# Performance work log

Measured on AMD Instinct MI355X. Metric: run time of the kernel, lower is better.

The kernel has to match this reference:

```python
import jax, jax.numpy as jnp
import numpy as np
from jax import lax

# ---- static config (matches init_kwargs: input_shape=(1,64,64), num_classes=2) ----
C, H, W = 1, 64, 64
NUM_CLASSES = 2
DIM_CAPS = 8          # primary capsule dim
NUM_PRIM = 32         # primary capsule types
OUT_DIM = 16          # class capsule dim
NUM_ROUTING = 3
HP = (H - 9) // 2 + 1  # 28  (9x9 conv, stride 2, no pad)
WP = (W - 9) // 2 + 1  # 28
IN_CAPS = NUM_PRIM * HP * WP  # 25088
TEMP_CH = 256 // H    # 4  channels after re-viewing temporal output
B = 32


def conv1d(x, w, b, pad):
    y = lax.conv_general_dilated(x, w, (1,), [(pad, pad)],
                                 dimension_numbers=('NCH', 'OIH', 'NCH'))
    return y + b[None, :, None]


def conv2d(x, w, b, stride, pad):
    y = lax.conv_general_dilated(x, w, (stride, stride), [(pad, pad), (pad, pad)],
                                 dimension_numbers=('NCHW', 'OIHW', 'NCHW'))
    return y + b[None, :, None, None]


def squash_vec(u):
    # proper capsule squash over last (dim_caps) axis -- used by PrimaryCapsule
    sn = jnp.sum(u * u, axis=-1, keepdims=True)
    return sn * u / ((1.0 + sn) * jnp.sqrt(sn + 1e-8))


def squash_elem(v):
    # RoutingCapsule squash: torch applies it over a trailing SINGLETON dim,
    # so it is elementwise: v^2 * v / ((1+v^2) * sqrt(v^2 + 1e-8))
    sn = v * v
    return sn * v / ((1.0 + sn) * jnp.sqrt(sn + 1e-8))


def setup_inputs() -> dict:
    key = jax.random.key(0)
    ks = jax.random.split(key, 20)
    s = 0.05
    inp = {
        'x':    jax.random.normal(ks[0], (B, C, H, W), dtype=jnp.float32),
        # temporal Conv1d stack (true in_channels = C*H = 64)
        'w_t1': jax.random.normal(ks[1], (64, C * H, 5), jnp.float32) * s,
        'b_t1': jnp.zeros((64,), jnp.float32),
        'w_t2': jax.random.normal(ks[2], (128, 64, 5), jnp.float32) * s,
        'b_t2': jnp.zeros((128,), jnp.float32),
        'w_t3': jax.random.normal(ks[3], (256, 128, 5), jnp.float32) * s,
        'b_t3': jnp.zeros((256,), jnp.float32),
        # spectral Conv2d stack
        'w_s1': jax.random.normal(ks[4], (64, C, 3, 3), jnp.float32) * s,
        'b_s1': jnp.zeros((64,), jnp.float32),
        'w_s2': jax.random.normal(ks[5], (128, 64, 3, 3), jnp.float32) * s,
        'b_s2': jnp.zeros((128,), jnp.float32),
        'w_s3': jax.random.normal(ks[6], (256, 128, 3, 3), jnp.float32) * s,
        'b_s3': jnp.zeros((256,), jnp.float32),
        # fusion 1x1 conv (in = 256/H + 256 = 260)
        'w_f':  jax.random.normal(ks[7], (256, TEMP_CH + 256, 1, 1), jnp.float32) * s,
        'b_f':  jnp.zeros((256,), jnp.float32),
        # primary capsule 9x9 stride-2 conv (out = 32*8 = 256)
        'w_p':  jax.random.normal(ks[8], (NUM_PRIM * DIM_CAPS, 256, 9, 9), jnp.float32) * s,
        'b_p':  jnp.zeros((NUM_PRIM * DIM_CAPS,), jnp.float32),
        # routing weight (torch: (1, in_caps, out_caps, out_dim, in_dim); leading 1 dropped)
        'w_r':  jax.random.normal(ks[9], (IN_CAPS, NUM_CLASSES, OUT_DIM, DIM_CAPS), jnp.float32) * s,
    }
    return inp


def reference(x, w_t1, b_t1, w_t2, b_t2, w_t3, b_t3,
              w_s1, b_s1, w_s2, b_s2, w_s3, b_s3,
              w_f, b_f, w_p, b_p, w_r):
    bsz = x.shape[0]
    # temporal branch: (B, C*H, W) -> Conv1d x3 -> (B, 256, W) -> (B, 256/H, H, W)
    xt = x.reshape(bsz, C * H, W)
    t = jax.nn.relu(conv1d(xt, w_t1, b_t1, 2))
    t = jax.nn.relu(conv1d(t, w_t2, b_t2, 2))
    t = jax.nn.relu(conv1d(t, w_t3, b_t3, 2))
    t = t.reshape(bsz, TEMP_CH, H, W)
    # spectral branch
    sp = jax.nn.relu(conv2d(x, w_s1, b_s1, 1, 1))
    sp = jax.nn.relu(conv2d(sp, w_s2, b_s2, 1, 1))
    sp = jax.nn.relu(conv2d(sp, w_s3, b_s3, 1, 1))
    # fuse
    fused = jnp.concatenate([t, sp], axis=1)          # (B, 260, H, W)
    fused = conv2d(fused, w_f, b_f, 1, 0)             # (B, 256, H, W)
    # primary capsules
    p = conv2d(fused, w_p, b_p, 2, 0)                 # (B, 256, HP, WP)
    p = p.reshape(bsz, NUM_PRIM, DIM_CAPS, HP * WP)
    p = jnp.transpose(p, (0, 1, 3, 2)).reshape(bsz, IN_CAPS, DIM_CAPS)
    u = squash_vec(p)                                 # (B, in_caps, 8)
    # dynamic routing
    u_hat = jnp.einsum('iodk,bik->biod', w_r, u)      # (B, in_caps, out_caps, out_dim)
    b_ij = jnp.zeros((bsz, IN_CAPS, NUM_CLASSES), dtype=u_hat.dtype)
    v = None
    for it in range(NUM_ROUTING):
        c = jax.nn.softmax(b_ij, axis=2)              # over out_caps
        s_j = jnp.einsum('bio,biod->bod', c, u_hat)   # (B, out_caps, out_dim)
        v = squash_elem(s_j)                          # elementwise (singleton-dim squash)
        if it < NUM_ROUTING - 1:
            b_ij = b_ij + jnp.einsum('biod,bod->bio', u_hat, v)
    # class_probs = (class_caps**2).sum(-1)**0.5 over a SINGLETON dim -> |v|
    return (v * v) ** 0.5                             # (B, num_classes, out_dim)
```

## Files before the change

### kernel.cpp

```cpp
#include <hip/hip_runtime.h>
#include <math.h>


#define BSZ 32

typedef unsigned short u16;
using bf16x8 = __attribute__((ext_vector_type(8))) short;
using f16x8 = __attribute__((ext_vector_type(8))) _Float16;
using f32x4 = __attribute__((ext_vector_type(4))) float;

__device__ inline u16 f2bf(float f) {
  union { float f; unsigned u; } v; v.f = f;
  unsigned r = v.u + 0x7FFF + ((v.u >> 16) & 1);
  return (u16)(r >> 16);
}
__device__ inline float bf2f(u16 h) {
  union { unsigned u; float f; } v; v.u = ((unsigned)h) << 16;
  return v.f;
}
__device__ inline u16 f2h(float f) {
  union { _Float16 h; u16 u; } v; v.h = (_Float16)f;
  return v.u;
}
__device__ inline float h2f(u16 b) {
  union { u16 u; _Float16 h; } v; v.u = b;
  return (float)v.h;
}

__global__ __launch_bounds__(256) void conv1d_relu_k(
    const float* __restrict__ in, const float* __restrict__ w,
    const float* __restrict__ bias, float* __restrict__ out, int CI, int CO) {
  int idx = blockIdx.x * 256 + threadIdx.x;
  int total = BSZ * CO * 64;
  if (idx >= total) return;
  int x = idx & 63;
  int co = (idx >> 6) % CO;
  int b = idx / (64 * CO);
  const float* ip = in + (size_t)b * CI * 64;
  const float* wp = w + (size_t)co * CI * 5;
  float acc = bias[co];
  for (int ci = 0; ci < CI; ++ci) {
    const float* ir = ip + ci * 64;
    const float* wr_ = wp + ci * 5;
#pragma unroll
    for (int k = 0; k < 5; ++k) {
      int xx = x + k - 2;
      if (xx >= 0 && xx < 64) acc += ir[xx] * wr_[k];
    }
  }
  out[idx] = fmaxf(acc, 0.f);
}

template <int CI, int CIC>
__global__ __launch_bounds__(256) void conv3x3_relu_k(
    const float* __restrict__ in, const float* __restrict__ w,
    const float* __restrict__ bias, float* __restrict__ out, int CO) {
  __shared__ float in_t[CIC][18][20];
  __shared__ float w_t[CIC][16][12];
  int t = threadIdx.x;
  int co_l = t & 15;
  int g = t >> 4;
  int gy = g >> 2, gx = g & 3;
  int y0 = (blockIdx.x >> 2) * 16, x0 = (blockIdx.x & 3) * 16;
  int co = blockIdx.y * 16 + co_l;
  int b = blockIdx.z;
  float acc[16];
#pragma unroll
  for (int i = 0; i < 16; ++i) acc[i] = 0.f;

  for (int cib = 0; cib < CI / CIC; ++cib) {
    int ci0 = cib * CIC;
    for (int s = t; s < CIC * 324; s += 256) {
      int ci = s / 324;
      int r = s - ci * 324;
      int iy = r / 18, ix = r - iy * 18;
      int gyy = y0 + iy - 1, gxx = x0 + ix - 1;
      float v = 0.f;
      if (gyy >= 0 && gyy < 64 && gxx >= 0 && gxx < 64)
        v = in[((size_t)b * CI + ci0 + ci) * 4096 + gyy * 64 + gxx];
      in_t[ci][iy][ix] = v;
    }
    for (int s = t; s < CIC * 144; s += 256) {
      int ci = s / 144;
      int r = s - ci * 144;
      int cw = r / 9, k = r - cw * 9;
      w_t[ci][cw][k] = w[((size_t)(blockIdx.y * 16 + cw) * CI + ci0 + ci) * 9 + k];
    }
    __syncthreads();
    for (int ci = 0; ci < CIC; ++ci) {
      float wv[9];
#pragma unroll
      for (int k = 0; k < 9; ++k) wv[k] = w_t[ci][co_l][k];
      float pin[36];
#pragma unroll
      for (int r6 = 0; r6 < 6; ++r6)
#pragma unroll
        for (int c6 = 0; c6 < 6; ++c6)
          pin[r6 * 6 + c6] = in_t[ci][4 * gy + r6][4 * gx + c6];
#pragma unroll
      for (int py = 0; py < 4; ++py)
#pragma unroll
        for (int px = 0; px < 4; ++px) {
          float s_ = acc[py * 4 + px];
#pragma unroll
          for (int ky = 0; ky < 3; ++ky)
#pragma unroll
            for (int kx = 0; kx < 3; ++kx)
              s_ += pin[(py + ky) * 6 + (px + kx)] * wv[ky * 3 + kx];
          acc[py * 4 + px] = s_;
        }
    }
    __syncthreads();
  }
  float bv = bias[co];
#pragma unroll
  for (int py = 0; py < 4; ++py)
#pragma unroll
    for (int px = 0; px < 4; ++px)
      out[((size_t)b * CO + co) * 4096 + (size_t)(y0 + 4 * gy + py) * 64 +
          (x0 + 4 * gx + px)] = fmaxf(acc[py * 4 + px] + bv, 0.f);
}

__global__ __launch_bounds__(256) void transpose_wf1_k(const float* __restrict__ wf,
                                                       u16* __restrict__ wh,
                                                       u16* __restrict__ wl) {
  int c = blockIdx.x;
  int co = threadIdx.x;
  u16 th[32], tl[32];
#pragma unroll
  for (int j = 0; j < 32; ++j) {
    int lc = c * 32 + j;
    float f = (lc < 260) ? wf[(size_t)co * 260 + lc] : 0.f;
    u16 h = f2bf(f);
    th[j] = h;
    tl[j] = f2bf(f - bf2f(h));
  }
  ushort4* dh = (ushort4*)(wh + ((size_t)c * 256 + co) * 32);
  ushort4* dl = (ushort4*)(wl + ((size_t)c * 256 + co) * 32);
#pragma unroll
  for (int q = 0; q < 8; ++q) {
    dh[q] = make_ushort4(th[4 * q], th[4 * q + 1], th[4 * q + 2], th[4 * q + 3]);
    dl[q] = make_ushort4(tl[4 * q], tl[4 * q + 1], tl[4 * q + 2], tl[4 * q + 3]);
  }
}

__global__ __launch_bounds__(256) void transpose_wp_k(const float* __restrict__ wp,
                                                      u16* __restrict__ wth,
                                                      u16* __restrict__ wtl) {
  int s = blockIdx.x;
  int g = s / 81, t = s - g * 81;
  int co = threadIdx.x;
  u16 th[32], tl[32];
#pragma unroll
  for (int c = 0; c < 32; ++c) {
    float f = wp[((size_t)co * 256 + g * 32 + c) * 81 + t];
    u16 h = f2h(f);
    th[c] = h;
    tl[c] = f2h(f - h2f(h));
  }
  ushort4* dh = (ushort4*)(wth + ((size_t)s * 256 + co) * 32);
  ushort4* dl = (ushort4*)(wtl + ((size_t)s * 256 + co) * 32);
#pragma unroll
  for (int q = 0; q < 8; ++q) {
    dh[q] = make_ushort4(th[4 * q], th[4 * q + 1], th[4 * q + 2], th[4 * q + 3]);
    dl[q] = make_ushort4(tl[4 * q], tl[4 * q + 1], tl[4 * q + 2], tl[4 * q + 3]);
  }
}

template <int CO, int NCHUNK>
__global__ __launch_bounds__(256) void transpose_w3_k(const float* __restrict__ w,
                                                      u16* __restrict__ wh,
                                                      u16* __restrict__ wl) {
  int tab = blockIdx.x;
  int g = tab / 9, tap = tab - g * 9;
  int co = threadIdx.x;
  if (co >= CO) return;
  constexpr int CI = NCHUNK * 32;
  u16 th[32], tl[32];
#pragma unroll
  for (int c = 0; c < 32; ++c) {
    float f = w[((size_t)co * CI + g * 32 + c) * 9 + tap];
    u16 h = f2bf(f);
    th[c] = h;
    tl[c] = f2bf(f - bf2f(h));
  }
  ushort4* dh = (ushort4*)(wh + ((size_t)tab * CO + co) * 32);
  ushort4* dl = (ushort4*)(wl + ((size_t)tab * CO + co) * 32);
#pragma unroll
  for (int q = 0; q < 8; ++q) {
    dh[q] = make_ushort4(th[4 * q], th[4 * q + 1], th[4 * q + 2], th[4 * q + 3]);
    dl[q] = make_ushort4(tl[4 * q], tl[4 * q + 1], tl[4 * q + 2], tl[4 * q + 3]);
  }
}

template <int WMG, int WNG, int NCHUNK, int CO>
__global__ __launch_bounds__(512) void conv3x3_mfma_k(const float* __restrict__ in,
                                                      const u16* __restrict__ Wh,
                                                      const u16* __restrict__ Wl,
                                                      const float* __restrict__ bias,
                                                      float* __restrict__ out) {
  constexpr int CI = NCHUNK * 32;
  constexpr int ROWS = WMG + 2;
  __shared__ __align__(16) char lds_a[ROWS * 66 * 80];
  const int tid = threadIdx.x;
  const int b = blockIdx.y;
  const int y0 = blockIdx.x * WMG;
  const int w = tid >> 6, l = tid & 63;
  const int wm = w / WNG, wn = w % WNG;
  const int kb = l >> 4, il = l & 15;

  int abase[4];
#pragma unroll
  for (int mb = 0; mb < 4; ++mb) {
    int lp = (wm * 4 + mb) * 16 + il;
    int ly = lp >> 6, lx = lp & 63;
    abase[mb] = (ly * 66 + lx) * 80 + kb * 16;
  }
  int boff[4];
#pragma unroll
  for (int nbi = 0; nbi < 4; ++nbi)
    boff[nbi] = ((wn * 4 + nbi) * 16 + il) * 64 + kb * 16;

  f32x4 acc[4][4];
#pragma unroll
  for (int mb = 0; mb < 4; ++mb)
#pragma unroll
    for (int nbi = 0; nbi < 4; ++nbi) {
      f32x4 z = {0.f, 0.f, 0.f, 0.f};
      acc[mb][nbi] = z;
    }

  const float* Fb = in + (size_t)b * CI * 4096;
  const char* WhB = (const char*)Wh;
  const char* WlB = (const char*)Wl;

  auto stageA = [&](int g, int plane) {
    const float* src = Fb + (size_t)g * 32 * 4096;
    for (int s = tid; s < ROWS * 66 * 8; s += 512) {
      int ciq = s & 7;
      int rest = s >> 3;
      int r = rest / 66, x = rest - r * 66;
      int row = y0 - 1 + r, col = x - 1;
      float a0 = 0.f, a1 = 0.f, a2 = 0.f, a3 = 0.f;
      if (row >= 0 && row < 64 && col >= 0 && col < 64) {
        const float* p = src + (size_t)(ciq * 4) * 4096 + row * 64 + col;
        a0 = p[0];
        a1 = p[4096];
        a2 = p[8192];
        a3 = p[12288];
      }
      u16 e0, e1, e2, e3;
      if (plane == 0) {
        e0 = f2bf(a0); e1 = f2bf(a1); e2 = f2bf(a2); e3 = f2bf(a3);
      } else {
        u16 h0 = f2bf(a0), h1 = f2bf(a1), h2 = f2bf(a2), h3 = f2bf(a3);
        e0 = f2bf(a0 - bf2f(h0)); e1 = f2bf(a1 - bf2f(h1));
        e2 = f2bf(a2 - bf2f(h2)); e3 = f2bf(a3 - bf2f(h3));
      }
      *(ushort4*)(lds_a + (r * 66 + x) * 80 + ciq * 8) = make_ushort4(e0, e1, e2, e3);
    }
  };

  for (int g = 0; g < NCHUNK; ++g) {
    __syncthreads();
    stageA(g, 0);
    __syncthreads();
#pragma unroll
    for (int tap = 0; tap < 9; ++tap) {
      const char* pb = WhB + (size_t)(g * 9 + tap) * (CO * 64);
      const char* pl = WlB + (size_t)(g * 9 + tap) * (CO * 64);
      bf16x8 bh[4], bl[4];
#pragma unroll
      for (int nbi = 0; nbi < 4; ++nbi) {
        bh[nbi] = *(const bf16x8*)(pb + boff[nbi]);
        bl[nbi] = *(const bf16x8*)(pl + boff[nbi]);
      }
      int ky = tap / 3, kx = tap - ky * 3;
      int toff = (ky * 66 + kx) * 80;
      bf16x8 av[4];
#pragma unroll
      for (int mb = 0; mb < 4; ++mb)
        av[mb] = *(const bf16x8*)(lds_a + abase[mb] + toff);
#pragma unroll
      for (int mb = 0; mb < 4; ++mb)
#pragma unroll
        for (int nbi = 0; nbi < 4; ++nbi) {
          acc[mb][nbi] = __builtin_amdgcn_mfma_f32_16x16x32_bf16(
              av[mb], bh[nbi], acc[mb][nbi], 0, 0, 0);
          acc[mb][nbi] = __builtin_amdgcn_mfma_f32_16x16x32_bf16(
              av[mb], bl[nbi], acc[mb][nbi], 0, 0, 0);
        }
    }
    __syncthreads();
    stageA(g, 1);
    __syncthreads();
#pragma unroll
    for (int tap = 0; tap < 9; ++tap) {
      const char* pb = WhB + (size_t)(g * 9 + tap) * (CO * 64);
      bf16x8 bh[4];
#pragma unroll
      for (int nbi = 0; nbi < 4; ++nbi)
        bh[nbi] = *(const bf16x8*)(pb + boff[nbi]);
      int ky = tap / 3, kx = tap - ky * 3;
      int toff = (ky * 66 + kx) * 80;
      bf16x8 av[4];
#pragma unroll
      for (int mb = 0; mb < 4; ++mb)
        av[mb] = *(const bf16x8*)(lds_a + abase[mb] + toff);
#pragma unroll
      for (int mb = 0; mb < 4; ++mb)
#pragma unroll
        for (int nbi = 0; nbi < 4; ++nbi)
          acc[mb][nbi] = __builtin_amdgcn_mfma_f32_16x16x32_bf16(
              av[mb], bh[nbi], acc[mb][nbi], 0, 0, 0);
    }
  }

  const int p0 = y0 * 64;
#pragma unroll
  for (int mb = 0; mb < 4; ++mb) {
    int pixb = p0 + (wm * 4 + mb) * 16 + kb * 4;
#pragma unroll
    for (int nbi = 0; nbi < 4; ++nbi) {
      int co = (wn * 4 + nbi) * 16 + il;
      float bv_ = bias[co];
      f32x4 a = acc[mb][nbi];
      float4 o = make_float4(fmaxf(a[0] + bv_, 0.f), fmaxf(a[1] + bv_, 0.f),
                             fmaxf(a[2] + bv_, 0.f), fmaxf(a[3] + bv_, 0.f));
      *(float4*)(out + (size_t)(b * CO + co) * 4096 + pixb) = o;
    }
  }
}

__global__ __launch_bounds__(512) void fuse_mfma_k(const float* __restrict__ t3,
                                                   const u16* __restrict__ Wh,
                                                   const u16* __restrict__ Wl,
                                                   const float* __restrict__ bf,
                                                   float* __restrict__ a) {
  constexpr int APL = 128 * 80;
  __shared__ __align__(16) char lds_a[2 * APL];
  const int tid = threadIdx.x;
  const int b = blockIdx.y;
  const int p0 = blockIdx.x * 128;
  const int w = tid >> 6, l = tid & 63;
  const int wm = w >> 2, wn = w & 3;
  const int kb = l >> 4, il = l & 15;

  int abase[4];
#pragma unroll
  for (int mb = 0; mb < 4; ++mb)
    abase[mb] = ((wm * 4 + mb) * 16 + il) * 80 + kb * 16;
  int boff[4];
#pragma unroll
  for (int nbi = 0; nbi < 4; ++nbi)
    boff[nbi] = ((wn * 4 + nbi) * 16 + il) * 64 + kb * 16;

  f32x4 acc[4][4];
#pragma unroll
  for (int mb = 0; mb < 4; ++mb)
#pragma unroll
    for (int nbi = 0; nbi < 4; ++nbi) {
      f32x4 z = {0.f, 0.f, 0.f, 0.f};
      acc[mb][nbi] = z;
    }

  const char* WhB = (const char*)Wh;
  const char* WlB = (const char*)Wl;

  auto stageAB = [&](int c) {
    for (int s = tid; s < 128 * 8; s += 512) {
      int ciq = s & 7, px = s >> 3;
      int pg = p0 + px;
      u16 eh[4], el[4];
#pragma unroll
      for (int q = 0; q < 4; ++q) {
        int lc = c * 32 + ciq * 4 + q;
        float f = 0.f;
        if (lc < 4)
          f = t3[(size_t)b * 16384 + lc * 4096 + pg];
        else if (lc < 260)
          f = a[((size_t)b * 256 + (lc - 4)) * 4096 + pg];
        u16 h = f2bf(f);
        eh[q] = h;
        el[q] = f2bf(f - bf2f(h));
      }
      *(ushort4*)(lds_a + px * 80 + ciq * 8) = make_ushort4(eh[0], eh[1], eh[2], eh[3]);
      *(ushort4*)(lds_a + APL + px * 80 + ciq * 8) =
          make_ushort4(el[0], el[1], el[2], el[3]);
    }
  };

  for (int c = 0; c < 9; ++c) {
    __syncthreads();
    stageAB(c);
    __syncthreads();
    bf16x8 bh[4], bl[4];
#pragma unroll
    for (int nbi = 0; nbi < 4; ++nbi) {
      bh[nbi] = *(const bf16x8*)(WhB + (size_t)c * 16384 + boff[nbi]);
      bl[nbi] = *(const bf16x8*)(WlB + (size_t)c * 16384 + boff[nbi]);
    }
    bf16x8 avh[4], avl[4];
#pragma unroll
    for (int mb = 0; mb < 4; ++mb) {
      avh[mb] = *(const bf16x8*)(lds_a + abase[mb]);
      avl[mb] = *(const bf16x8*)(lds_a + APL + abase[mb]);
    }
#pragma unroll
    for (int mb = 0; mb < 4; ++mb)
#pragma unroll
      for (int nbi = 0; nbi < 4; ++nbi) {
        acc[mb][nbi] = __builtin_amdgcn_mfma_f32_16x16x32_bf16(
            avh[mb], bh[nbi], acc[mb][nbi], 0, 0, 0);
        acc[mb][nbi] = __builtin_amdgcn_mfma_f32_16x16x32_bf16(
            avh[mb], bl[nbi], acc[mb][nbi], 0, 0, 0);
        acc[mb][nbi] = __builtin_amdgcn_mfma_f32_16x16x32_bf16(
            avl[mb], bh[nbi], acc[mb][nbi], 0, 0, 0);
      }
  }

#pragma unroll
  for (int mb = 0; mb < 4; ++mb) {
    int pixb = p0 + (wm * 4 + mb) * 16 + kb * 4;
#pragma unroll
    for (int nbi = 0; nbi < 4; ++nbi) {
      int co = (wn * 4 + nbi) * 16 + il;
      float bv_ = bf[co];
      f32x4 v = acc[mb][nbi];
      float4 o = make_float4(v[0] + bv_, v[1] + bv_, v[2] + bv_, v[3] + bv_);
      *(float4*)(a + (size_t)(b * 256 + co) * 4096 + pixb) = o;
    }
  }
}

__global__ __launch_bounds__(1024) void conv9x9_mfma_k(const float* __restrict__ fused,
                                                       const u16* __restrict__ WTh,
                                                       const u16* __restrict__ WTl,
                                                       const float* __restrict__ bias,
                                                       float* __restrict__ praw) {
  constexpr int APLANE = 19 * 32 * 80;
  __shared__ __align__(16) char lds_a[2 * APLANE];
  const int tid = threadIdx.x;
  const int b = blockIdx.y, tile = blockIdx.x;
  const int p0 = tile * 128;
  const int oy0 = p0 / 28;
  const int w = tid >> 6, l = tid & 63;
  const int wm = w >> 3, wn = w & 7;
  const int kb = l >> 4, il = l & 15;

  int abase[4];
#pragma unroll
  for (int mb = 0; mb < 4; ++mb) {
    int p = p0 + (wm * 4 + mb) * 16 + il;
    int oy = p / 28, ox = p - oy * 28;
    abase[mb] = (2 * (oy - oy0)) * 2560 + ox * 80 + kb * 16;
  }
  int boff[2];
#pragma unroll
  for (int nbi = 0; nbi < 2; ++nbi)
    boff[nbi] = (wn * 32 + nbi * 16 + il) * 64 + kb * 16;

  f32x4 acc[4][2];
#pragma unroll
  for (int mb = 0; mb < 4; ++mb)
#pragma unroll
    for (int nbi = 0; nbi < 2; ++nbi) {
      f32x4 z = {0.f, 0.f, 0.f, 0.f};
      acc[mb][nbi] = z;
    }

  const float* Fb = fused + (size_t)b * 256 * 4096;
  const char* WhB = (const char*)WTh;
  const char* WlB = (const char*)WTl;

  auto stageA = [&](int g) {
    const float* src = Fb + (size_t)g * 32 * 4096;
    for (int s = tid; s < 19 * 63 * 8; s += 1024) {
      int ciq = s / 1197;
      int rem = s - ciq * 1197;
      int r = rem / 63, t63 = rem - r * 63;
      int x2 = (t63 < 32) ? 2 * t63 : 2 * (t63 - 32) + 1;
      int iy = 2 * oy0 + r;
      float a0 = 0.f, a1 = 0.f, a2 = 0.f, a3 = 0.f;
      if (iy < 64) {
        const float* pp0 = src + (size_t)(ciq * 4) * 4096 + iy * 64 + x2;
        a0 = pp0[0];
        a1 = pp0[4096];
        a2 = pp0[8192];
        a3 = pp0[12288];
      }
      u16 e0 = f2h(a0), e1 = f2h(a1), e2 = f2h(a2), e3 = f2h(a3);
      int off = (x2 & 1) * APLANE + (r * 32 + (x2 >> 1)) * 80 + ciq * 8;
      *(ushort4*)(lds_a + off) = make_ushort4(e0, e1, e2, e3);
    }
  };

  for (int g = 0; g < 8; ++g) {
    __syncthreads();
    stageA(g);
    __syncthreads();
#pragma unroll 3
    for (int t = 0; t < 81; ++t) {
      const char* pb = WhB + (size_t)(g * 81 + t) * 16384;
      const char* pl = WlB + (size_t)(g * 81 + t) * 16384;
      f16x8 bh[2], bl[2];
#pragma unroll
      for (int nbi = 0; nbi < 2; ++nbi) {
        bh[nbi] = *(const f16x8*)(pb + boff[nbi]);
        bl[nbi] = *(const f16x8*)(pl + boff[nbi]);
      }
      int ky = t / 9, kx = t - ky * 9;
      int toff = (kx & 1) * APLANE + ky * 2560 + (kx >> 1) * 80;
      f16x8 av[4];
#pragma unroll
      for (int mb = 0; mb < 4; ++mb)
        av[mb] = *(const f16x8*)(lds_a + abase[mb] + toff);
#pragma unroll
      for (int mb = 0; mb < 4; ++mb)
#pragma unroll
        for (int nbi = 0; nbi < 2; ++nbi) {
          acc[mb][nbi] = __builtin_amdgcn_mfma_f32_16x16x32_f16(
              av[mb], bh[nbi], acc[mb][nbi], 0, 0, 0);
          acc[mb][nbi] = __builtin_amdgcn_mfma_f32_16x16x32_f16(
              av[mb], bl[nbi], acc[mb][nbi], 0, 0, 0);
        }
    }
  }

#pragma unroll
  for (int mb = 0; mb < 4; ++mb) {
    int pixb = p0 + (wm * 4 + mb) * 16 + kb * 4;
    if (pixb < 784) {
#pragma unroll
      for (int nbi = 0; nbi < 2; ++nbi) {
        int co = wn * 32 + nbi * 16 + il;
        float bv_ = bias[co];
        f32x4 v = acc[mb][nbi];
        float4 o = make_float4(v[0] + bv_, v[1] + bv_, v[2] + bv_, v[3] + bv_);
        *(float4*)(praw + (size_t)(b * 256 + co) * 784 + pixb) = o;
      }
    }
  }
}

__global__ __launch_bounds__(256) void squash_uhat_k(const float* __restrict__ praw,
                                                     const float* __restrict__ w_r,
                                                     float* __restrict__ u_hat) {
  int i = blockIdx.x * 256 + threadIdx.x;
  int b = blockIdx.y;
  int prim = i / 784, pix = i - prim * 784;
  const float* pp = praw + ((size_t)b * 256 + prim * 8) * 784 + pix;
  float xv[8];
  float sn = 0.f;
#pragma unroll
  for (int d = 0; d < 8; ++d) {
    xv[d] = pp[(size_t)d * 784];
    sn += xv[d] * xv[d];
  }
  float scale = sn / ((1.f + sn) * sqrtf(sn + 1e-8f));
  float4 ua = make_float4(xv[0] * scale, xv[1] * scale, xv[2] * scale, xv[3] * scale);
  float4 ub = make_float4(xv[4] * scale, xv[5] * scale, xv[6] * scale, xv[7] * scale);

  const float4* wr = (const float4*)(w_r + (size_t)i * 256);
  float res[32];
#pragma unroll
  for (int od = 0; od < 32; ++od) {
    float4 wa = wr[od * 2], wb = wr[od * 2 + 1];
    res[od] = wa.x * ua.x + wa.y * ua.y + wa.z * ua.z + wa.w * ua.w +
              wb.x * ub.x + wb.y * ub.y + wb.z * ub.z + wb.w * ub.w;
  }
  float4* dst = (float4*)(u_hat + ((size_t)b * 25088 + i) * 32);
#pragma unroll
  for (int q = 0; q < 8; ++q)
    dst[q] = make_float4(res[4 * q], res[4 * q + 1], res[4 * q + 2], res[4 * q + 3]);
}

__global__ __launch_bounds__(256) void route_sj_k(const float* __restrict__ u_hat,
                                                  float* __restrict__ sj_part) {
  int b = blockIdx.x;
  int seg = blockIdx.y;
  int t = threadIdx.x;
  float acc[32];
#pragma unroll
  for (int j = 0; j < 32; ++j) acc[j] = 0.f;
  int i0 = seg * 3136;
  for (int i = i0 + t; i < i0 + 3136; i += 256) {
    const float4* uh = (const float4*)(u_hat + ((size_t)b * 25088 + i) * 32);
#pragma unroll
    for (int q = 0; q < 4; ++q) {
      float4 va = uh[q];
      acc[4 * q + 0] += 0.5f * va.x;
      acc[4 * q + 1] += 0.5f * va.y;
      acc[4 * q + 2] += 0.5f * va.z;
      acc[4 * q + 3] += 0.5f * va.w;
      float4 vb = uh[4 + q];
      acc[16 + 4 * q + 0] += 0.5f * vb.x;
      acc[16 + 4 * q + 1] += 0.5f * vb.y;
      acc[16 + 4 * q + 2] += 0.5f * vb.z;
      acc[16 + 4 * q + 3] += 0.5f * vb.w;
    }
  }
#pragma unroll
  for (int j = 0; j < 32; ++j) {
    acc[j] += __shfl_down(acc[j], 32);
    acc[j] += __shfl_down(acc[j], 16);
    acc[j] += __shfl_down(acc[j], 8);
    acc[j] += __shfl_down(acc[j], 4);
    acc[j] += __shfl_down(acc[j], 2);
    acc[j] += __shfl_down(acc[j], 1);
  }
  __shared__ float red[4][32];
  int wave = t >> 6, lane = t & 63;
  if (lane == 0) {
#pragma unroll
    for (int j = 0; j < 32; ++j) red[wave][j] = acc[j];
  }
  __syncthreads();
  if (t < 32) {
    float s = red[0][t] + red[1][t] + red[2][t] + red[3][t];
    sj_part[((size_t)b * 8 + seg) * 32 + t] = s;
  }
}

__global__ __launch_bounds__(256) void route_fsj_k(const float* __restrict__ u_hat,
                                                   const float* __restrict__ v,
                                                   float* __restrict__ b_ij,
                                                   float* __restrict__ sj_part, int first) {
  int b = blockIdx.x;
  int seg = blockIdx.y;
  int t = threadIdx.x;
  float4 vp[8];
  const float4* vv = (const float4*)(v + b * 32);
#pragma unroll
  for (int q = 0; q < 8; ++q) vp[q] = vv[q];
  float acc[32];
#pragma unroll
  for (int j = 0; j < 32; ++j) acc[j] = 0.f;
  int i0 = seg * 3136;
  for (int i = i0 + t; i < i0 + 3136; i += 256) {
    const float4* uhp = (const float4*)(u_hat + ((size_t)b * 25088 + i) * 32);
    float4 uh[8];
#pragma unroll
    for (int q = 0; q < 8; ++q) uh[q] = uhp[q];
    float e0 = 0.f, e1 = 0.f;
#pragma unroll
    for (int q = 0; q < 4; ++q) {
      e0 += uh[q].x * vp[q].x + uh[q].y * vp[q].y + uh[q].z * vp[q].z + uh[q].w * vp[q].w;
      e1 += uh[4 + q].x * vp[4 + q].x + uh[4 + q].y * vp[4 + q].y +
            uh[4 + q].z * vp[4 + q].z + uh[4 + q].w * vp[4 + q].w;
    }
    size_t o = ((size_t)b * 25088 + i) * 2;
    float b0, b1;
    if (first) {
      b0 = e0;
      b1 = e1;
      b_ij[o + 0] = e0;
      b_ij[o + 1] = e1;
    } else {
      b0 = b_ij[o + 0] + e0;
      b1 = b_ij[o + 1] + e1;
    }
    float m = fmaxf(b0, b1);
    float x0 = expf(b0 - m), x1 = expf(b1 - m);
    float inv = 1.f / (x0 + x1);
    float c0 = x0 * inv, c1 = x1 * inv;
#pragma unroll
    for (int q = 0; q < 4; ++q) {
      acc[4 * q + 0] += c0 * uh[q].x;
      acc[4 * q + 1] += c0 * uh[q].y;
      acc[4 * q + 2] += c0 * uh[q].z;
      acc[4 * q + 3] += c0 * uh[q].w;
      acc[16 + 4 * q + 0] += c1 * uh[4 + q].x;
      acc[16 + 4 * q + 1] += c1 * uh[4 + q].y;
      acc[16 + 4 * q + 2] += c1 * uh[4 + q].z;
      acc[16 + 4 * q + 3] += c1 * uh[4 + q].w;
    }
  }
#pragma unroll
  for (int j = 0; j < 32; ++j) {
    acc[j] += __shfl_down(acc[j], 32);
    acc[j] += __shfl_down(acc[j], 16);
    acc[j] += __shfl_down(acc[j], 8);
    acc[j] += __shfl_down(acc[j], 4);
    acc[j] += __shfl_down(acc[j], 2);
    acc[j] += __shfl_down(acc[j], 1);
  }
  __shared__ float red[4][32];
  int wave = t >> 6, lane = t & 63;
  if (lane == 0) {
#pragma unroll
    for (int j = 0; j < 32; ++j) red[wave][j] = acc[j];
  }
  __syncthreads();
  if (t < 32) {
    float s = red[0][t] + red[1][t] + red[2][t] + red[3][t];
    sj_part[((size_t)b * 8 + seg) * 32 + t] = s;
  }
}

__global__ __launch_bounds__(256) void route_fin_k(const float* __restrict__ sj_part,
                                                   float* __restrict__ v,
                                                   float* __restrict__ out, int final_it) {
  int idx = blockIdx.x * 256 + threadIdx.x;
  if (idx >= BSZ * 32) return;
  int b = idx >> 5, j = idx & 31;
  float s = 0.f;
#pragma unroll
  for (int seg = 0; seg < 8; ++seg) s += sj_part[((size_t)b * 8 + seg) * 32 + j];
  float sn = s * s;
  float vv = sn * s / ((1.f + sn) * sqrtf(sn + 1e-8f));
  v[idx] = vv;
  if (final_it) out[idx] = fabsf(vv);
}

extern "C" void kernel_launch(void* const* d_in, const int* in_sizes, int n_in,
                              void* d_out, int out_size, void* d_ws, size_t ws_size,
                              hipStream_t stream) {
  (void)in_sizes; (void)n_in; (void)out_size;
  const float* x    = (const float*)d_in[0];
  const float* w_t1 = (const float*)d_in[1];
  const float* b_t1 = (const float*)d_in[2];
  const float* w_t2 = (const float*)d_in[3];
  const float* b_t2 = (const float*)d_in[4];
  const float* w_t3 = (const float*)d_in[5];
  const float* b_t3 = (const float*)d_in[6];
  const float* w_s1 = (const float*)d_in[7];
  const float* b_s1 = (const float*)d_in[8];
  const float* w_s2 = (const float*)d_in[9];
  const float* b_s2 = (const float*)d_in[10];
  const float* w_s3 = (const float*)d_in[11];
  const float* b_s3 = (const float*)d_in[12];
  const float* w_f  = (const float*)d_in[13];
  const float* b_f  = (const float*)d_in[14];
  const float* w_p  = (const float*)d_in[15];
  const float* b_p  = (const float*)d_in[16];
  const float* w_r  = (const float*)d_in[17];
  float* out = (float*)d_out;

  char* ws = (char*)d_ws;
  if (ws_size < 238854144ull) return;
  float* fused = (float*)(ws + 0);
  float* uhat  = (float*)(ws + 0);
  float* s2q   = (float*)(ws + 134217728);
  float* praw  = (float*)(ws + 134217728);
  float* b_ij  = (float*)(ws + 185597952);
  float* s1    = (float*)(ws + 201326592);
  float* t1    = (float*)(ws + 201326592);
  float* t2    = (float*)(ws + 201850880);
  float* t3    = (float*)(ws + 202899456);
  u16*   wTh   = (u16*)  (ws + 204996608);
  u16*   wTl   = (u16*)  (ws + 215613440);
  u16*   w3a_h = (u16*)  (ws + 234881024);
  u16*   w3a_l = (u16*)  (ws + 235028480);
  u16*   w3b_h = (u16*)  (ws + 235175936);
  u16*   w3b_l = (u16*)  (ws + 235765760);
  u16*   wf1_h = (u16*)  (ws + 236355584);
  u16*   wf1_l = (u16*)  (ws + 236503040);
  float* sjp   = (float*)(ws + 236650496);
  float* vbuf  = (float*)(ws + 236683264);

  transpose_w3_k<128, 2><<<18, 256, 0, stream>>>(w_s2, w3a_h, w3a_l);
  transpose_w3_k<256, 4><<<36, 256, 0, stream>>>(w_s3, w3b_h, w3b_l);
  transpose_wf1_k<<<9, 256, 0, stream>>>(w_f, wf1_h, wf1_l);

  conv3x3_relu_k<1, 1><<<dim3(16, 4, BSZ), 256, 0, stream>>>(x, w_s1, b_s1, s1, 64);
  conv3x3_mfma_k<4, 2, 2, 128><<<dim3(16, BSZ), 512, 0, stream>>>(s1, w3a_h, w3a_l, b_s2, s2q);

  conv1d_relu_k<<<512, 256, 0, stream>>>(x, w_t1, b_t1, t1, 64, 64);
  conv1d_relu_k<<<1024, 256, 0, stream>>>(t1, w_t2, b_t2, t2, 64, 128);
  conv1d_relu_k<<<2048, 256, 0, stream>>>(t2, w_t3, b_t3, t3, 128, 256);
  transpose_wp_k<<<648, 256, 0, stream>>>(w_p, wTh, wTl);

  conv3x3_mfma_k<2, 4, 4, 256><<<dim3(32, BSZ), 512, 0, stream>>>(s2q, w3b_h, w3b_l, b_s3, fused);

  fuse_mfma_k<<<dim3(32, BSZ), 512, 0, stream>>>(t3, wf1_h, wf1_l, b_f, fused);

  conv9x9_mfma_k<<<dim3(7, BSZ), 1024, 0, stream>>>(fused, wTh, wTl, b_p, praw);

  squash_uhat_k<<<dim3(98, BSZ), 256, 0, stream>>>(praw, w_r, uhat);

  route_sj_k<<<dim3(BSZ, 8), 256, 0, stream>>>(uhat, sjp);
  route_fin_k<<<4, 256, 0, stream>>>(sjp, vbuf, out, 0);
  route_fsj_k<<<dim3(BSZ, 8), 256, 0, stream>>>(uhat, vbuf, b_ij, sjp, 1);
  route_fin_k<<<4, 256, 0, stream>>>(sjp, vbuf, out, 0);
  route_fsj_k<<<dim3(BSZ, 8), 256, 0, stream>>>(uhat, vbuf, b_ij, sjp, 0);
  route_fin_k<<<4, 256, 0, stream>>>(sjp, vbuf, out, 1);
}
```

Baseline: 1.566 ms.

## Fuse temporal conv stack, merge hi/lo staging passes, fold squash into routing

Replaces the three conv1d launches with a single per-batch kernel that keeps the intermediates in shared memory. The 3x3 MFMA conv now stages the hi and lo bf16 planes together in a double-size LDS buffer and issues all three split-precision MFMAs in one pass, which halves the staging and synchronisation work. The routing squash step is folded into the next routing kernel, removing two small launches. The risk is that the fused temporal kernel runs only 32 blocks, which may underuse the GPU, and the larger LDS buffer may reduce occupancy of the conv kernel.

```diff
diff --git a/kernel.cpp b/kernel.cpp
--- a/kernel.cpp
+++ b/kernel.cpp
@@ -27,28 +27,66 @@
   return (float)v.h;
 }
 
-__global__ __launch_bounds__(256) void conv1d_relu_k(
-    const float* __restrict__ in, const float* __restrict__ w,
-    const float* __restrict__ bias, float* __restrict__ out, int CI, int CO) {
-  int idx = blockIdx.x * 256 + threadIdx.x;
-  int total = BSZ * CO * 64;
-  if (idx >= total) return;
-  int x = idx & 63;
-  int co = (idx >> 6) % CO;
-  int b = idx / (64 * CO);
-  const float* ip = in + (size_t)b * CI * 64;
-  const float* wp = w + (size_t)co * CI * 5;
-  float acc = bias[co];
-  for (int ci = 0; ci < CI; ++ci) {
-    const float* ir = ip + ci * 64;
-    const float* wr_ = wp + ci * 5;
-#pragma unroll
-    for (int k = 0; k < 5; ++k) {
-      int xx = x + k - 2;
-      if (xx >= 0 && xx < 64) acc += ir[xx] * wr_[k];
-    }
-  }
-  out[idx] = fmaxf(acc, 0.f);
+__global__ __launch_bounds__(256) void temporal_k(
+    const float* __restrict__ x,
+    const float* __restrict__ w1, const float* __restrict__ b1,
+    const float* __restrict__ w2, const float* __restrict__ b2,
+    const float* __restrict__ w3, const float* __restrict__ b3,
+    float* __restrict__ t3out) {
+  __shared__ float s_in[64 * 64];
+  __shared__ float s_t1[64 * 64];
+  __shared__ float s_t2[128 * 64];
+  const int b = blockIdx.x;
+  const int tid = threadIdx.x;
+  for (int s = tid; s < 4096; s += 256) s_in[s] = x[(size_t)b * 4096 + s];
+  __syncthreads();
+  for (int s = tid; s < 4096; s += 256) {
+    int co = s >> 6, xx = s & 63;
+    float acc = b1[co];
+    const float* wp = w1 + (size_t)co * 320;
+    for (int ci = 0; ci < 64; ++ci) {
+      const float* ir = s_in + ci * 64;
+      const float* wr_ = wp + ci * 5;
+#pragma unroll
+      for (int k = 0; k < 5; ++k) {
+        int p = xx + k - 2;
+        if (p >= 0 && p < 64) acc += ir[p] * wr_[k];
+      }
+    }
+    s_t1[s] = fmaxf(acc, 0.f);
+  }
+  __syncthreads();
+  for (int s = tid; s < 8192; s += 256) {
+    int co = s >> 6, xx = s & 63;
+    float acc = b2[co];
+    const float* wp = w2 + (size_t)co * 320;
+    for (int ci = 0; ci < 64; ++ci) {
+      const float* ir = s_t1 + ci * 64;
+      const float* wr_ = wp + ci * 5;
+#pragma unroll
+      for (int k = 0; k < 5; ++k) {
+        int p = xx + k - 2;
+        if (p >= 0 && p < 64) acc += ir[p] * wr_[k];
+      }
+    }
+    s_t2[s] = fmaxf(acc, 0.f);
+  }
+  __syncthreads();
+  for (int s = tid; s < 16384; s += 256) {
+    int co = s >> 6, xx = s & 63;
+    float acc = b3[co];
+    const float* wp = w3 + (size_t)co * 640;
+    for (int ci = 0; ci < 128; ++ci) {
+      const float* ir = s_t2 + ci * 64;
+      const float* wr_ = wp + ci * 5;
+#pragma unroll
+      for (int k = 0; k < 5; ++k) {
+        int p = xx + k - 2;
+        if (p >= 0 && p < 64) acc += ir[p] * wr_[k];
+      }
+    }
+    t3out[(size_t)b * 16384 + s] = fmaxf(acc, 0.f);
+  }
 }
 
 template <int CI, int CIC>
@@ -201,7 +239,8 @@
                                                       float* __restrict__ out) {
   constexpr int CI = NCHUNK * 32;
   constexpr int ROWS = WMG + 2;
-  __shared__ __align__(16) char lds_a[ROWS * 66 * 80];
+  constexpr int APL = ROWS * 66 * 80;
+  __shared__ __align__(16) char lds_a[2 * APL];
   const int tid = threadIdx.x;
   const int b = blockIdx.y;
   const int y0 = blockIdx.x * WMG;
@@ -234,7 +273,7 @@
   const char* WhB = (const char*)Wh;
   const char* WlB = (const char*)Wl;
 
-  auto stageA = [&](int g, int plane) {
+  auto stageA2 = [&](int g) {
     const float* src = Fb + (size_t)g * 32 * 4096;
     for (int s = tid; s < ROWS * 66 * 8; s += 512) {
       int ciq = s & 7;
@@ -249,21 +288,18 @@
         a2 = p[8192];
         a3 = p[12288];
       }
-      u16 e0, e1, e2, e3;
-      if (plane == 0) {
-        e0 = f2bf(a0); e1 = f2bf(a1); e2 = f2bf(a2); e3 = f2bf(a3);
-      } else {
-        u16 h0 = f2bf(a0), h1 = f2bf(a1), h2 = f2bf(a2), h3 = f2bf(a3);
-        e0 = f2bf(a0 - bf2f(h0)); e1 = f2bf(a1 - bf2f(h1));
-        e2 = f2bf(a2 - bf2f(h2)); e3 = f2bf(a3 - bf2f(h3));
-      }
-      *(ushort4*)(lds_a + (r * 66 + x) * 80 + ciq * 8) = make_ushort4(e0, e1, e2, e3);
+      u16 h0 = f2bf(a0), h1 = f2bf(a1), h2 = f2bf(a2), h3 = f2bf(a3);
+      u16 l0 = f2bf(a0 - bf2f(h0)), l1 = f2bf(a1 - bf2f(h1));
+      u16 l2 = f2bf(a2 - bf2f(h2)), l3 = f2bf(a3 - bf2f(h3));
+      int off = (r * 66 + x) * 80 + ciq * 8;
+      *(ushort4*)(lds_a + off) = make_ushort4(h0, h1, h2, h3);
+      *(ushort4*)(lds_a + APL + off) = make_ushort4(l0, l1, l2, l3);
     }
   };
 
   for (int g = 0; g < NCHUNK; ++g) {
     __syncthreads();
-    stageA(g, 0);
+    stageA2(g);
     __syncthreads();
 #pragma unroll
     for (int tap = 0; tap < 9; ++tap) {
@@ -277,42 +313,23 @@
       }
       int ky = tap / 3, kx = tap - ky * 3;
       int toff = (ky * 66 + kx) * 80;
-      bf16x8 av[4];
-#pragma unroll
-      for (int mb = 0; mb < 4; ++mb)
-        av[mb] = *(const bf16x8*)(lds_a + abase[mb] + toff);
+      bf16x8 avh[4], avl[4];
+#pragma unroll
+      for (int mb = 0; mb < 4; ++mb) {
+        avh[mb] = *(const bf16x8*)(lds_a + abase[mb] + toff);
+        avl[mb] = *(const bf16x8*)(lds_a + APL + abase[mb] + toff);
+      }
 #pragma unroll
       for (int mb = 0; mb < 4; ++mb)
 #pragma unroll
         for (int nbi = 0; nbi < 4; ++nbi) {
           acc[mb][nbi] = __builtin_amdgcn_mfma_f32_16x16x32_bf16(
-              av[mb], bh[nbi], acc[mb][nbi], 0, 0, 0);
+              avh[mb], bh[nbi], acc[mb][nbi], 0, 0, 0);
           acc[mb][nbi] = __builtin_amdgcn_mfma_f32_16x16x32_bf16(
-              av[mb], bl[nbi], acc[mb][nbi], 0, 0, 0);
+              avh[mb], bl[nbi], acc[mb][nbi], 0, 0, 0);
+          acc[mb][nbi] = __builtin_amdgcn_mfma_f32_16x16x32_bf16(
+              avl[mb], bh[nbi], acc[mb][nbi], 0, 0, 0);
         }
-    }
-    __syncthreads();
-    stageA(g, 1);
-    __syncthreads();
-#pragma unroll
-    for (int tap = 0; tap < 9; ++tap) {
-      const char* pb = WhB + (size_t)(g * 9 + tap) * (CO * 64);
-      bf16x8 bh[4];
-#pragma unroll
-      for (int nbi = 0; nbi < 4; ++nbi)
-        bh[nbi] = *(const bf16x8*)(pb + boff[nbi]);
-      int ky = tap / 3, kx = tap - ky * 3;
-      int toff = (ky * 66 + kx) * 80;
-      bf16x8 av[4];
-#pragma unroll
-      for (int mb = 0; mb < 4; ++mb)
-        av[mb] = *(const bf16x8*)(lds_a + abase[mb] + toff);
-#pragma unroll
-      for (int mb = 0; mb < 4; ++mb)
-#pragma unroll
-        for (int nbi = 0; nbi < 4; ++nbi)
-          acc[mb][nbi] = __builtin_amdgcn_mfma_f32_16x16x32_bf16(
-              av[mb], bh[nbi], acc[mb][nbi], 0, 0, 0);
     }
   }
 
@@ -623,16 +640,25 @@
 }
 
 __global__ __launch_bounds__(256) void route_fsj_k(const float* __restrict__ u_hat,
-                                                   const float* __restrict__ v,
+                                                   const float* __restrict__ sjp_in,
                                                    float* __restrict__ b_ij,
-                                                   float* __restrict__ sj_part, int first) {
+                                                   float* __restrict__ sjp_out, int first) {
   int b = blockIdx.x;
   int seg = blockIdx.y;
   int t = threadIdx.x;
-  float4 vp[8];
-  const float4* vv = (const float4*)(v + b * 32);
-#pragma unroll
-  for (int q = 0; q < 8; ++q) vp[q] = vv[q];
+  __shared__ float vsh[32];
+  if (t < 32) {
+    float s = 0.f;
+#pragma unroll
+    for (int sg = 0; sg < 8; ++sg) s += sjp_in[((size_t)b * 8 + sg) * 32 + t];
+    float sn = s * s;
+    vsh[t] = sn * s / ((1.f + sn) * sqrtf(sn + 1e-8f));
+  }
+  __syncthreads();
+  float vp[32];
+#pragma unroll
+  for (int j = 0; j < 32; ++j) vp[j] = vsh[j];
+
   float acc[32];
 #pragma unroll
   for (int j = 0; j < 32; ++j) acc[j] = 0.f;
@@ -645,9 +671,10 @@
     float e0 = 0.f, e1 = 0.f;
 #pragma unroll
     for (int q = 0; q < 4; ++q) {
-      e0 += uh[q].x * vp[q].x + uh[q].y * vp[q].y + uh[q].z * vp[q].z + uh[q].w * vp[q].w;
-      e1 += uh[4 + q].x * vp[4 + q].x + uh[4 + q].y * vp[4 + q].y +
-            uh[4 + q].z * vp[4 + q].z + uh[4 + q].w * vp[4 + q].w;
+      e0 += uh[q].x * vp[4 * q] + uh[q].y * vp[4 * q + 1] + uh[q].z * vp[4 * q + 2] +
+            uh[q].w * vp[4 * q + 3];
+      e1 += uh[4 + q].x * vp[16 + 4 * q] + uh[4 + q].y * vp[16 + 4 * q + 1] +
+            uh[4 + q].z * vp[16 + 4 * q + 2] + uh[4 + q].w * vp[16 + 4 * q + 3];
     }
     size_t o = ((size_t)b * 25088 + i) * 2;
     float b0, b1;
@@ -694,7 +721,7 @@
   __syncthreads();
   if (t < 32) {
     float s = red[0][t] + red[1][t] + red[2][t] + red[3][t];
-    sj_part[((size_t)b * 8 + seg) * 32 + t] = s;
+    sjp_out[((size_t)b * 8 + seg) * 32 + t] = s;
   }
 }
 
@@ -745,8 +772,6 @@
   float* praw  = (float*)(ws + 134217728);
   float* b_ij  = (float*)(ws + 185597952);
   float* s1    = (float*)(ws + 201326592);
-  float* t1    = (float*)(ws + 201326592);
-  float* t2    = (float*)(ws + 201850880);
   float* t3    = (float*)(ws + 202899456);
   u16*   wTh   = (u16*)  (ws + 204996608);
   u16*   wTl   = (u16*)  (ws + 215613440);
@@ -756,8 +781,9 @@
   u16*   w3b_l = (u16*)  (ws + 235765760);
   u16*   wf1_h = (u16*)  (ws + 236355584);
   u16*   wf1_l = (u16*)  (ws + 236503040);
-  float* sjp   = (float*)(ws + 236650496);
-  float* vbuf  = (float*)(ws + 236683264);
+  float* sjpA  = (float*)(ws + 236650496);
+  float* sjpB  = (float*)(ws + 236683264);
+  float* vbuf  = (float*)(ws + 236716032);
 
   transpose_w3_k<128, 2><<<18, 256, 0, stream>>>(w_s2, w3a_h, w3a_l);
   transpose_w3_k<256, 4><<<36, 256, 0, stream>>>(w_s3, w3b_h, w3b_l);
@@ -766,9 +792,7 @@
   conv3x3_relu_k<1, 1><<<dim3(16, 4, BSZ), 256, 0, stream>>>(x, w_s1, b_s1, s1, 64);
   conv3x3_mfma_k<4, 2, 2, 128><<<dim3(16, BSZ), 512, 0, stream>>>(s1, w3a_h, w3a_l, b_s2, s2q);
 
-  conv1d_relu_k<<<512, 256, 0, stream>>>(x, w_t1, b_t1, t1, 64, 64);
-  conv1d_relu_k<<<1024, 256, 0, stream>>>(t1, w_t2, b_t2, t2, 64, 128);
-  conv1d_relu_k<<<2048, 256, 0, stream>>>(t2, w_t3, b_t3, t3, 128, 256);
+  temporal_k<<<BSZ, 256, 0, stream>>>(x, w_t1, b_t1, w_t2, b_t2, w_t3, b_t3, t3);
   transpose_wp_k<<<648, 256, 0, stream>>>(w_p, wTh, wTl);
 
   conv3x3_mfma_k<2, 4, 4, 256><<<dim3(32, BSZ), 512, 0, stream>>>(s2q, w3b_h, w3b_l, b_s3, fused);
@@ -779,10 +803,8 @@
 
   squash_uhat_k<<<dim3(98, BSZ), 256, 0, stream>>>(praw, w_r, uhat);
 
-  route_sj_k<<<dim3(BSZ, 8), 256, 0, stream>>>(uhat, sjp);
-  route_fin_k<<<4, 256, 0, stream>>>(sjp, vbuf, out, 0);
-  route_fsj_k<<<dim3(BSZ, 8), 256, 0, stream>>>(uhat, vbuf, b_ij, sjp, 1);
-  route_fin_k<<<4, 256, 0, stream>>>(sjp, vbuf, out, 0);
-  route_fsj_k<<<dim3(BSZ, 8), 256, 0, stream>>>(uhat, vbuf, b_ij, sjp, 0);
-  route_fin_k<<<4, 256, 0, stream>>>(sjp, vbuf, out, 1);
-}
+  route_sj_k<<<dim3(BSZ, 8), 256, 0, stream>>>(uhat, sjpA);
+  route_fsj_k<<<dim3(BSZ, 8), 256, 0, stream>>>(uhat, sjpA, b_ij, sjpB, 1);
+  route_fsj_k<<<dim3(BSZ, 8), 256, 0, stream>>>(uhat, sjpB, b_ij, sjpA, 0);
+  route_fin_k<<<4, 256, 0, stream>>>(sjpA, vbuf, out, 1);
+}
```

Measured after the change: 5.043 ms. 3.22x slower.
